# Performance work log

Hardware: AMD Instinct MI355X
Metric: run time of the kernel (lower is better)

## Reference

```python
import jax, jax.numpy as jnp
import numpy as np

B, D = 1048576, 64  # batch, series length


def _expit_m1(t):
    # R -> (-1, 1)
    return 2.0 * jax.nn.sigmoid(t) - 1.0


def _precision_ar1(param, dim):
    # Tridiagonal AR(1) precision: I + coef * (superdiag + subdiag)
    p = _expit_m1(param)                      # shape (1,)
    coef = -p / (1.0 + p ** 2)                # shape (1,)
    off = jnp.eye(dim, k=1) + jnp.eye(dim, k=-1)
    return jnp.eye(dim) + coef * off          # (dim, dim)


def setup_inputs() -> dict:
    key = jax.random.key(0)
    k1, k2, k3 = jax.random.split(key, 3)
    y_true = jax.random.normal(k1, (B, D), dtype=jnp.float32)
    y_pred = jax.random.normal(k2, (B, D), dtype=jnp.float32)
    # per-row valid lengths in [1, D] (avoid 0 to keep out/n finite)
    n = jax.random.randint(k3, (B,), 1, D + 1)
    param = jnp.zeros((1,), dtype=jnp.float32)  # nn.Parameter(torch.zeros(1))
    return {"y_true": y_true, "y_pred": y_pred, "param": param, "n": n}


def reference(y_true, y_pred, param, n):
    dim = y_true.shape[-1]
    # filter_by_n: zero out positions t >= n[b]
    mask = (jnp.arange(dim)[None, :] < n[:, None]).astype(y_true.dtype)
    diff = (y_true - y_pred) * mask           # (B, D)
    P = _precision_ar1(param, dim)            # (D, D)
    # diag(diff @ P @ diff.T) computed as batched quadratic form, O(B*D^2)
    quad = jnp.einsum('bi,ij,bj->b', diff, P, diff)  # (B,)
    return jnp.mean(quad / n.astype(y_true.dtype))
```

## Files before the change

### kernel.cpp

```cpp
#include <hip/hip_runtime.h>

#define BLOCK 256
#define UNROLL 8
#define CHUNK (BLOCK * UNROLL)

__global__ __launch_bounds__(BLOCK) void mahal_main(
    const float4* __restrict__ yt4,
    const float4* __restrict__ yp4,
    const float*  __restrict__ param,
    const int*    __restrict__ n,
    float* __restrict__ partial,
    int total_vec4)
{
    float t = param[0];
    float p = 2.0f / (1.0f + __expf(-t)) - 1.0f;
    float coef2 = -2.0f * p / (1.0f + p * p);

    int base = blockIdx.x * CHUNK + (int)threadIdx.x;

    float4 a[UNROLL], b[UNROLL];
    int    vv[UNROLL];

    if ((blockIdx.x + 1) * CHUNK <= total_vec4) {
        #pragma unroll
        for (int j = 0; j < UNROLL; ++j) {
            int g = base + j * BLOCK;
            a[j]  = yt4[g];
            b[j]  = yp4[g];
            vv[j] = n[g >> 4];
        }
    } else {
        #pragma unroll
        for (int j = 0; j < UNROLL; ++j) {
            int gj = base + j * BLOCK;
            int g  = gj < total_vec4 ? gj : 0;
            a[j]  = yt4[g];
            b[j]  = yp4[g];
            vv[j] = (gj < total_vec4) ? n[g >> 4] : 0;
        }
    }
    __builtin_amdgcn_sched_barrier(0);

    int col4 = threadIdx.x & 15;
    int e0   = col4 << 2;
    bool not_last = (col4 != 15);
    float acc = 0.0f;

    #pragma unroll
    for (int j = 0; j < UNROLL; ++j) {
        int v = vv[j];
        float d0 = (e0 + 0 < v) ? (a[j].x - b[j].x) : 0.0f;
        float d1 = (e0 + 1 < v) ? (a[j].y - b[j].y) : 0.0f;
        float d2 = (e0 + 2 < v) ? (a[j].z - b[j].z) : 0.0f;
        float d3 = (e0 + 3 < v) ? (a[j].w - b[j].w) : 0.0f;
        float nb = __shfl_down(d0, 1, 64);
        float sumsq = d0 * d0 + d1 * d1 + d2 * d2 + d3 * d3;
        float cross = d0 * d1 + d1 * d2 + d2 * d3;
        if (not_last) cross += d3 * nb;
        float q  = fmaf(coef2, cross, sumsq);
        float rv = __builtin_amdgcn_rcpf((float)(v > 0 ? v : 1));
        acc = fmaf(q, rv, acc);
    }

    #pragma unroll
    for (int off = 32; off >= 1; off >>= 1)
        acc += __shfl_down(acc, off, 64);

    __shared__ float smem[BLOCK / 64];
    int lane = threadIdx.x & 63;
    int wid  = threadIdx.x >> 6;
    if (lane == 0) smem[wid] = acc;
    __syncthreads();
    if (threadIdx.x == 0) {
        float s = 0.0f;
        #pragma unroll
        for (int i = 0; i < BLOCK / 64; ++i) s += smem[i];
        partial[blockIdx.x] = s;
    }
}

__global__ __launch_bounds__(256) void mahal_finish(
    const float* __restrict__ partial,
    float* __restrict__ out,
    int nblocks, float invB)
{
    float acc = 0.0f;
    if ((nblocks & 3) == 0) {
        const float4* p4 = (const float4*)partial;
        int n4 = nblocks >> 2;
        for (int i = threadIdx.x; i < n4; i += 256) {
            float4 v = p4[i];
            acc += v.x + v.y + v.z + v.w;
        }
    } else {
        for (int i = threadIdx.x; i < nblocks; i += 256)
            acc += partial[i];
    }
    #pragma unroll
    for (int off = 32; off >= 1; off >>= 1)
        acc += __shfl_down(acc, off, 64);
    __shared__ float smem[4];
    int lane = threadIdx.x & 63;
    int wid  = threadIdx.x >> 6;
    if (lane == 0) smem[wid] = acc;
    __syncthreads();
    if (threadIdx.x == 0)
        out[0] = (smem[0] + smem[1] + smem[2] + smem[3]) * invB;
}

extern "C" void kernel_launch(void* const* d_in, const int* in_sizes, int n_in,
                              void* d_out, int out_size, void* d_ws, size_t ws_size,
                              hipStream_t stream) {
    const float* y_true = (const float*)d_in[0];
    const float* y_pred = (const float*)d_in[1];
    const float* param  = (const float*)d_in[2];
    const int*   n      = (const int*)d_in[3];
    float* out = (float*)d_out;

    int total = in_sizes[0];
    int B     = in_sizes[3];
    int total_vec4 = total / 4;
    float invB = 1.0f / (float)B;

    int blocks = (total_vec4 + CHUNK - 1) / CHUNK;
    float* partial = (float*)d_ws;

    mahal_main<<<blocks, BLOCK, 0, stream>>>((const float4*)y_true,
                                             (const float4*)y_pred,
                                             param, n, partial, total_vec4);
    mahal_finish<<<1, 256, 0, stream>>>(partial, out, blocks, invB);
}
```

Baseline: 505.1 us.

## Stage float4 loads through LDS with global_load_lds and halve per-block unroll

Full blocks now use direct global-to-LDS loads (16-byte global_load_lds) to bring y_true and y_pred into shared memory, then read them back after a barrier, instead of loading into registers. The per-block chunk is halved (UNROLL 8 to 4), so the grid doubles in blocks. The aim is to cut register pressure and raise occupancy and memory-level parallelism in this bandwidth-bound streaming reduction. The cost is 32 KB of LDS per block, which may itself limit occupancy, plus an extra barrier and LDS round trip.

```diff
diff --git a/kernel.cpp b/kernel.cpp
--- a/kernel.cpp
+++ b/kernel.cpp
@@ -1,8 +1,8 @@
 #include <hip/hip_runtime.h>
 
-#define BLOCK 256
-#define UNROLL 8
-#define CHUNK (BLOCK * UNROLL)
+#define BLOCK  256
+#define UNROLL 4
+#define CHUNK4 (BLOCK * UNROLL)
 
 __global__ __launch_bounds__(BLOCK) void mahal_main(
     const float4* __restrict__ yt4,
@@ -12,54 +12,79 @@
     float* __restrict__ partial,
     int total_vec4)
 {
+    __shared__ float4 sA[CHUNK4];
+    __shared__ float4 sB[CHUNK4];
+
     float t = param[0];
     float p = 2.0f / (1.0f + __expf(-t)) - 1.0f;
     float coef2 = -2.0f * p / (1.0f + p * p);
 
-    int base = blockIdx.x * CHUNK + (int)threadIdx.x;
+    const int tid  = threadIdx.x;
+    const int wave = tid >> 6;
+    const int lane = tid & 63;
+    const int gbase = blockIdx.x * CHUNK4;
 
-    float4 a[UNROLL], b[UNROLL];
-    int    vv[UNROLL];
+    const int col4 = tid & 15;
+    const int e0   = col4 << 2;
+    const bool not_last = (col4 != 15);
+    float acc = 0.0f;
 
-    if ((blockIdx.x + 1) * CHUNK <= total_vec4) {
+    if (gbase + CHUNK4 <= total_vec4) {
+        int vv[UNROLL];
         #pragma unroll
         for (int j = 0; j < UNROLL; ++j) {
-            int g = base + j * BLOCK;
-            a[j]  = yt4[g];
-            b[j]  = yp4[g];
-            vv[j] = n[g >> 4];
+            int k = j * BLOCK + wave * 64;
+            __builtin_amdgcn_global_load_lds(
+                (const __attribute__((address_space(1))) void*)(yt4 + gbase + k + lane),
+                (__attribute__((address_space(3))) void*)(&sA[k]), 16, 0, 0);
+            __builtin_amdgcn_global_load_lds(
+                (const __attribute__((address_space(1))) void*)(yp4 + gbase + k + lane),
+                (__attribute__((address_space(3))) void*)(&sB[k]), 16, 0, 0);
+        }
+        #pragma unroll
+        for (int j = 0; j < UNROLL; ++j)
+            vv[j] = n[(gbase + j * BLOCK + tid) >> 4];
+
+        __syncthreads();
+
+        #pragma unroll
+        for (int j = 0; j < UNROLL; ++j) {
+            int k = j * BLOCK + tid;
+            float4 a = sA[k];
+            float4 b = sB[k];
+            int v = vv[j];
+            float d0 = (e0 + 0 < v) ? (a.x - b.x) : 0.0f;
+            float d1 = (e0 + 1 < v) ? (a.y - b.y) : 0.0f;
+            float d2 = (e0 + 2 < v) ? (a.z - b.z) : 0.0f;
+            float d3 = (e0 + 3 < v) ? (a.w - b.w) : 0.0f;
+            float nb = __shfl_down(d0, 1, 64);
+            float sumsq = d0 * d0 + d1 * d1 + d2 * d2 + d3 * d3;
+            float cross = d0 * d1 + d1 * d2 + d2 * d3;
+            if (not_last) cross += d3 * nb;
+            float q  = fmaf(coef2, cross, sumsq);
+            float rv = __builtin_amdgcn_rcpf((float)(v > 0 ? v : 1));
+            acc = fmaf(q, rv, acc);
         }
     } else {
         #pragma unroll
         for (int j = 0; j < UNROLL; ++j) {
-            int gj = base + j * BLOCK;
-            int g  = gj < total_vec4 ? gj : 0;
-            a[j]  = yt4[g];
-            b[j]  = yp4[g];
-            vv[j] = (gj < total_vec4) ? n[g >> 4] : 0;
+            int g = gbase + j * BLOCK + tid;
+            int v = 0;
+            float4 a = make_float4(0.f, 0.f, 0.f, 0.f);
+            float4 b = a;
+            if (g < total_vec4) { a = yt4[g]; b = yp4[g]; v = n[g >> 4]; }
+            float d0 = (e0 + 0 < v) ? (a.x - b.x) : 0.0f;
+            float d1 = (e0 + 1 < v) ? (a.y - b.y) : 0.0f;
+            float d2 = (e0 + 2 < v) ? (a.z - b.z) : 0.0f;
+            float d3 = (e0 + 3 < v) ? (a.w - b.w) : 0.0f;
+            float nb = __shfl_down(d0, 1, 64);
+            float sumsq = d0 * d0 + d1 * d1 + d2 * d2 + d3 * d3;
+            float cross = d0 * d1 + d1 * d2 + d2 * d3;
+            if (not_last) cross += d3 * nb;
+            float q  = fmaf(coef2, cross, sumsq);
+            float rv = __builtin_amdgcn_rcpf((float)(v > 0 ? v : 1));
+            acc = fmaf(q, rv, acc);
         }
-    }
-    __builtin_amdgcn_sched_barrier(0);
-
-    int col4 = threadIdx.x & 15;
-    int e0   = col4 << 2;
-    bool not_last = (col4 != 15);
-    float acc = 0.0f;
-
-    #pragma unroll
-    for (int j = 0; j < UNROLL; ++j) {
-        int v = vv[j];
-        float d0 = (e0 + 0 < v) ? (a[j].x - b[j].x) : 0.0f;
-        float d1 = (e0 + 1 < v) ? (a[j].y - b[j].y) : 0.0f;
-        float d2 = (e0 + 2 < v) ? (a[j].z - b[j].z) : 0.0f;
-        float d3 = (e0 + 3 < v) ? (a[j].w - b[j].w) : 0.0f;
-        float nb = __shfl_down(d0, 1, 64);
-        float sumsq = d0 * d0 + d1 * d1 + d2 * d2 + d3 * d3;
-        float cross = d0 * d1 + d1 * d2 + d2 * d3;
-        if (not_last) cross += d3 * nb;
-        float q  = fmaf(coef2, cross, sumsq);
-        float rv = __builtin_amdgcn_rcpf((float)(v > 0 ? v : 1));
-        acc = fmaf(q, rv, acc);
     }
 
     #pragma unroll
@@ -67,11 +92,9 @@
         acc += __shfl_down(acc, off, 64);
 
     __shared__ float smem[BLOCK / 64];
-    int lane = threadIdx.x & 63;
-    int wid  = threadIdx.x >> 6;
-    if (lane == 0) smem[wid] = acc;
+    if (lane == 0) smem[wave] = acc;
     __syncthreads();
-    if (threadIdx.x == 0) {
+    if (tid == 0) {
         float s = 0.0f;
         #pragma unroll
         for (int i = 0; i < BLOCK / 64; ++i) s += smem[i];
@@ -122,7 +145,7 @@
     int total_vec4 = total / 4;
     float invB = 1.0f / (float)B;
 
-    int blocks = (total_vec4 + CHUNK - 1) / CHUNK;
+    int blocks = (total_vec4 + CHUNK4 - 1) / CHUNK4;
     float* partial = (float*)d_ws;
 
     mahal_main<<<blocks, BLOCK, 0, stream>>>((const float4*)y_true,
```

Measured after the change: 508.9 us. About the same (+0.7%).
